# Optimization experiments

Measured on AMD Instinct MI355X. Metric: run time of the kernel, lower is better.

## Reference

```python
import jax, jax.numpy as jnp
import numpy as np

D_MODEL = 1024
HEADS = 2
IDX_DIM = 32


def setup_inputs() -> dict:
    key = jax.random.key(0)
    kx, kq, kk, kw = jax.random.split(key, 4)
    x = jax.random.normal(kx, (2, 4096, D_MODEL), dtype=jnp.float32)
    # nn.Linear weights stored as [in, out] for direct x @ W
    scale = 1.0 / np.sqrt(D_MODEL)
    Wq = jax.random.normal(kq, (D_MODEL, HEADS * IDX_DIM), dtype=jnp.float32) * scale
    Wk = jax.random.normal(kk, (D_MODEL, IDX_DIM), dtype=jnp.float32) * scale
    Ww = jax.random.normal(kw, (D_MODEL, HEADS), dtype=jnp.float32) * scale
    return {"x": x, "Wq": Wq, "Wk": Wk, "Ww": Ww}


def reference(x, Wq, Wk, Ww):
    b, t, _ = x.shape
    queries = (x @ Wq).reshape(b, t, HEADS, IDX_DIM)   # [b,t,h,d]
    keys = x @ Wk                                       # [b,s,d]
    weights = x @ Ww                                    # [b,t,h]
    dots = jnp.einsum('bthd,bsd->bths', queries, keys)  # [b,t,h,s]
    activated = jax.nn.relu(dots)
    # per-head weight then reduce over heads -> [b,t,s]
    index_scores = jnp.einsum('bths,bth->bts', activated, weights)
    return index_scores
```

## Files before the change

kernel.cpp:

```cpp
#include <hip/hip_runtime.h>
#include <hip/hip_bf16.h>

#define DM    1024
#define NH    2
#define IDX   32
#define HQ    (NH*IDX)
#define TT    4096
#define BB    2
#define RR    (BB*TT)
#define NC    112
#define NTIL  7
#define SCW   512
#define SCH   (TT/SCW)

typedef short  s16x8 __attribute__((ext_vector_type(8)));
typedef float  f32x4 __attribute__((ext_vector_type(4)));

__device__ __forceinline__ unsigned short f2bf(float f) {
    unsigned int u = __builtin_bit_cast(unsigned int, f);
    u += 0x7FFFu + ((u >> 16) & 1u);
    return (unsigned short)(u >> 16);
}

__global__ __launch_bounds__(256) void prep_wcat(const float* __restrict__ Wq,
                                                 const float* __restrict__ Wk,
                                                 const float* __restrict__ Ww,
                                                 unsigned short* __restrict__ WcatT) {
    int idx = blockIdx.x * 256 + threadIdx.x;
    int j = idx >> 10;
    int i = idx & 1023;
    float v = 0.f;
    if (j < 64)       v = Wq[i * HQ + j];
    else if (j < 96)  v = Wk[i * IDX + (j - 64)];
    else if (j < 98)  v = Ww[i * NH + (j - 96)];
    WcatT[j * DM + i] = f2bf(v);
}

__global__ __launch_bounds__(256) void proj_kernel(const float* __restrict__ x,
                                                   const unsigned short* __restrict__ WcatT,
                                                   unsigned short* __restrict__ Qb,
                                                   unsigned short* __restrict__ Kb,
                                                   float* __restrict__ wb) {
    __shared__ float red[4][NTIL][64][4];

    const int wave = threadIdx.x >> 6;
    const int lane = threadIdx.x & 63;
    const int r0   = blockIdx.x * 16;
    const int lrow = lane & 15;
    const int lseg = lane >> 4;

    f32x4 acc[NTIL] = {};

    const float*          xr = x + (size_t)(r0 + lrow) * DM + wave * 256 + lseg * 8;
    const unsigned short* wr = WcatT + (size_t)lrow * DM + wave * 256 + lseg * 8;

    #pragma unroll 4
    for (int kc = 0; kc < 256; kc += 32) {
        float4 a0 = *(const float4*)(xr + kc);
        float4 a1 = *(const float4*)(xr + kc + 4);
        s16x8 af;
        af[0] = (short)f2bf(a0.x); af[1] = (short)f2bf(a0.y);
        af[2] = (short)f2bf(a0.z); af[3] = (short)f2bf(a0.w);
        af[4] = (short)f2bf(a1.x); af[5] = (short)f2bf(a1.y);
        af[6] = (short)f2bf(a1.z); af[7] = (short)f2bf(a1.w);
        #pragma unroll
        for (int t = 0; t < NTIL; ++t) {
            s16x8 bfv = *(const s16x8*)(wr + (size_t)t * 16 * DM + kc);
            acc[t] = __builtin_amdgcn_mfma_f32_16x16x32_bf16(af, bfv, acc[t], 0, 0, 0);
        }
    }

    #pragma unroll
    for (int t = 0; t < NTIL; ++t)
        *(f32x4*)&red[wave][t][lane][0] = acc[t];
    __syncthreads();

    #pragma unroll
    for (int u = 0; u < 2; ++u) {
        const int t = wave * 2 + u;
        if (t >= NTIL) break;
        f32x4 s = *(const f32x4*)&red[0][t][lane][0];
        s += *(const f32x4*)&red[1][t][lane][0];
        s += *(const f32x4*)&red[2][t][lane][0];
        s += *(const f32x4*)&red[3][t][lane][0];
        const int col = t * 16 + lrow;
        #pragma unroll
        for (int r = 0; r < 4; ++r) {
            int row = r0 + lseg * 4 + r;
            float v = s[r];
            if (col < 64)       Qb[(size_t)row * HQ + col]         = f2bf(v);
            else if (col < 96)  Kb[(size_t)row * IDX + (col - 64)] = f2bf(v);
            else if (col < 98)  wb[(size_t)row * NH + (col - 96)]  = v;
        }
    }
}

__global__ __launch_bounds__(256) void score_kernel(const unsigned short* __restrict__ Qb,
                                                    const unsigned short* __restrict__ Kb,
                                                    const float* __restrict__ wb,
                                                    float* __restrict__ out) {
    const int rb   = blockIdx.x >> 3;
    const int sc   = blockIdx.x & (SCH - 1);
    const int wave = threadIdx.x >> 6;
    const int lane = threadIdx.x & 63;
    const int trow = lane & 15;
    const int lseg = lane >> 4;

    const int t0 = rb * 64 + wave * 16;
    const int b  = t0 >> 12;

    const unsigned short* qrow = Qb + (size_t)(t0 + trow) * HQ + lseg * 8;
    s16x8 qb0 = *(const s16x8*)(qrow);
    s16x8 qb1 = *(const s16x8*)(qrow + IDX);

    float2 wt = *(const float2*)(wb + (size_t)(t0 + trow) * NH);

    const int s0 = sc * SCW;
    const unsigned short* kbase =
        Kb + ((size_t)(b * TT) + s0 + trow) * IDX + lseg * 8;
    float* obase = out + (size_t)(t0 + trow) * TT + s0 + lseg * 4;

    const f32x4 zero = {0.f, 0.f, 0.f, 0.f};

    #pragma unroll 4
    for (int it = 0; it < SCW / 16; ++it) {
        s16x8 kb = *(const s16x8*)(kbase + (size_t)it * 16 * IDX);
        f32x4 d0 = __builtin_amdgcn_mfma_f32_16x16x32_bf16(kb, qb0, zero, 0, 0, 0);
        f32x4 d1 = __builtin_amdgcn_mfma_f32_16x16x32_bf16(kb, qb1, zero, 0, 0, 0);
        f32x4 v;
        #pragma unroll
        for (int r = 0; r < 4; ++r)
            v[r] = wt.x * fmaxf(d0[r], 0.f) + wt.y * fmaxf(d1[r], 0.f);
        *(f32x4*)(obase + it * 16) = v;
    }
}

extern "C" void kernel_launch(void* const* d_in, const int* in_sizes, int n_in,
                              void* d_out, int out_size, void* d_ws, size_t ws_size,
                              hipStream_t stream) {
    const float* x  = (const float*)d_in[0];
    const float* Wq = (const float*)d_in[1];
    const float* Wk = (const float*)d_in[2];
    const float* Ww = (const float*)d_in[3];
    float* out = (float*)d_out;

    char* ws = (char*)d_ws;
    unsigned short* WcatT = (unsigned short*)ws;
    unsigned short* Qb    = (unsigned short*)(ws + 256 * 1024);
    unsigned short* Kb    = (unsigned short*)(ws + 256 * 1024 + 1024 * 1024);
    float*          wb    = (float*)(ws + 256 * 1024 + 1024 * 1024 + 512 * 1024);

    hipLaunchKernelGGL(prep_wcat, dim3((NC * DM) / 256), dim3(256), 0, stream,
                       Wq, Wk, Ww, WcatT);
    hipLaunchKernelGGL(proj_kernel, dim3(RR / 16), dim3(256), 0, stream,
                       x, WcatT, Qb, Kb, wb);
    hipLaunchKernelGGL(score_kernel, dim3((RR / 64) * SCH), dim3(256), 0, stream,
                       Qb, Kb, wb, out);
}
```

Measured before the change: 56.04 us.

## Stage x tile through swizzled LDS with coalesced loads in projection kernel

```diff
diff --git a/kernel.cpp b/kernel.cpp
--- a/kernel.cpp
+++ b/kernel.cpp
@@ -13,13 +13,13 @@
 #define SCW   512
 #define SCH   (TT/SCW)
 
+typedef short  s16x4 __attribute__((ext_vector_type(4)));
 typedef short  s16x8 __attribute__((ext_vector_type(8)));
 typedef float  f32x4 __attribute__((ext_vector_type(4)));
 
 __device__ __forceinline__ unsigned short f2bf(float f) {
-    unsigned int u = __builtin_bit_cast(unsigned int, f);
-    u += 0x7FFFu + ((u >> 16) & 1u);
-    return (unsigned short)(u >> 16);
+    __hip_bfloat16 h = __float2bfloat16(f);
+    return __builtin_bit_cast(unsigned short, h);
 }
 
 __global__ __launch_bounds__(256) void prep_wcat(const float* __restrict__ Wq,
@@ -41,48 +41,59 @@
                                                    unsigned short* __restrict__ Qb,
                                                    unsigned short* __restrict__ Kb,
                                                    float* __restrict__ wb) {
-    __shared__ float red[4][NTIL][64][4];
+    __shared__ __align__(16) unsigned char smem[32768];
 
-    const int wave = threadIdx.x >> 6;
-    const int lane = threadIdx.x & 63;
+    const int tid  = threadIdx.x;
+    const int wave = tid >> 6;
+    const int lane = tid & 63;
     const int r0   = blockIdx.x * 16;
     const int lrow = lane & 15;
     const int lseg = lane >> 4;
 
+    {
+        const float4* xsrc = (const float4*)(x + (size_t)r0 * DM);
+        #pragma unroll 8
+        for (int i = 0; i < 16; ++i) {
+            float4 a = xsrc[i * 256 + tid];
+            const int boff = i * 2048 + ((tid * 8) ^ ((i & 7) << 4));
+            s16x4 h;
+            h[0] = (short)f2bf(a.x); h[1] = (short)f2bf(a.y);
+            h[2] = (short)f2bf(a.z); h[3] = (short)f2bf(a.w);
+            *(s16x4*)(smem + boff) = h;
+        }
+    }
+    __syncthreads();
+
     f32x4 acc[NTIL] = {};
-
-    const float*          xr = x + (size_t)(r0 + lrow) * DM + wave * 256 + lseg * 8;
     const unsigned short* wr = WcatT + (size_t)lrow * DM + wave * 256 + lseg * 8;
 
-    #pragma unroll 4
-    for (int kc = 0; kc < 256; kc += 32) {
-        float4 a0 = *(const float4*)(xr + kc);
-        float4 a1 = *(const float4*)(xr + kc + 4);
-        s16x8 af;
-        af[0] = (short)f2bf(a0.x); af[1] = (short)f2bf(a0.y);
-        af[2] = (short)f2bf(a0.z); af[3] = (short)f2bf(a0.w);
-        af[4] = (short)f2bf(a1.x); af[5] = (short)f2bf(a1.y);
-        af[6] = (short)f2bf(a1.z); af[7] = (short)f2bf(a1.w);
+    #pragma unroll
+    for (int kc = 0; kc < 8; ++kc) {
+        const int boff = lrow * 2048 +
+            ((wave * 512 + kc * 64 + lseg * 16) ^ ((lrow & 7) << 4));
+        s16x8 af = *(const s16x8*)(smem + boff);
         #pragma unroll
         for (int t = 0; t < NTIL; ++t) {
-            s16x8 bfv = *(const s16x8*)(wr + (size_t)t * 16 * DM + kc);
+            s16x8 bfv = *(const s16x8*)(wr + (size_t)t * 16 * DM + kc * 32);
             acc[t] = __builtin_amdgcn_mfma_f32_16x16x32_bf16(af, bfv, acc[t], 0, 0, 0);
         }
     }
 
+    __syncthreads();
+    float* red = (float*)smem;
     #pragma unroll
     for (int t = 0; t < NTIL; ++t)
-        *(f32x4*)&red[wave][t][lane][0] = acc[t];
+        *(f32x4*)&red[(((wave * NTIL) + t) * 64 + lane) * 4] = acc[t];
     __syncthreads();
 
     #pragma unroll
     for (int u = 0; u < 2; ++u) {
-        const int t = wave * 2 + u;
+        const int t = wave + u * 4;
         if (t >= NTIL) break;
-        f32x4 s = *(const f32x4*)&red[0][t][lane][0];
-        s += *(const f32x4*)&red[1][t][lane][0];
-        s += *(const f32x4*)&red[2][t][lane][0];
-        s += *(const f32x4*)&red[3][t][lane][0];
+        f32x4 s = *(const f32x4*)&red[((0 * NTIL + t) * 64 + lane) * 4];
+        s += *(const f32x4*)&red[((1 * NTIL + t) * 64 + lane) * 4];
+        s += *(const f32x4*)&red[((2 * NTIL + t) * 64 + lane) * 4];
+        s += *(const f32x4*)&red[((3 * NTIL + t) * 64 + lane) * 4];
         const int col = t * 16 + lrow;
         #pragma unroll
         for (int r = 0; r < 4; ++r) {
```

Result: faster. 53.01 us (-5.4%).
